# Performance work log

Hardware: AMD Instinct MI355X
Metric: run time of the kernel (lower is better)

The kernel has to match this reference:

```python
import jax, jax.numpy as jnp
import numpy as np

B, CIN, COUT = 2, 32, 32
S = (16, 16, 16, 16)        # input spatial dims
K = (3, 3, 3, 3)            # kernel per spatial dim
PAD = (0, 0, 0, 0)          # conv-transpose padding


def setup_inputs() -> dict:
    key = jax.random.key(0)
    k1, k2, k3 = jax.random.split(key, 3)
    x = jax.random.normal(k1, (B, CIN) + S, dtype=jnp.float32)
    # weight layout mirrors torch ConvTranspose: (in_ch, out_ch, k0, k1, k2, k3)
    # (axis 2 indexes the per-frame sub-convolutions conv_layers[i] of the module)
    weight = jax.random.normal(k2, (CIN, COUT) + K, dtype=jnp.float32) * 0.05
    bias = jax.random.normal(k3, (COUT,), dtype=jnp.float32) * 0.05
    return {"x": x, "weight": weight, "bias": bias}


def _conv_transpose_4d(x, weight, bias):
    # stride-1 conv-transpose == regular conv with spatially flipped kernel
    # and per-side padding (k - 1 - p). This is exactly the math the original
    # module computes via its nested frame-accumulation loops (stride=1).
    w = jnp.flip(weight, axis=(2, 3, 4, 5))          # flip all spatial taps
    w = jnp.transpose(w, (1, 0, 2, 3, 4, 5))         # (O, I, k0..k3)
    pads = [(k - 1 - p, k - 1 - p) for k, p in zip(K, PAD)]
    dn = jax.lax.conv_dimension_numbers(x.shape, w.shape,
                                        ('NCWXYZ', 'OIWXYZ', 'NCWXYZ'))
    y = jax.lax.conv_general_dilated(
        x, w, window_strides=(1, 1, 1, 1), padding=pads,
        dimension_numbers=dn)
    # bias broadcast over batch + 4 spatial dims (module adds per out-channel)
    return y + bias[None, :, None, None, None, None]


def reference(x, weight, bias):
    return _conv_transpose_4d(x, weight, bias)
```

## Files before the change

### kernel.cpp

```cpp
#include <hip/hip_runtime.h>
#include <hip/hip_bf16.h>


#define B_    2
#define CIN_  32
#define SD    16
#define OD    18
#define NTAP  81
#define THREADS 256

typedef unsigned short u16;
typedef __attribute__((ext_vector_type(8))) short short8v;
typedef __attribute__((ext_vector_type(8))) unsigned short u16x8;
typedef __attribute__((ext_vector_type(16))) float f32x16;

__device__ inline u16 f2bf(float f) {
    unsigned u = __float_as_uint(f);
    u = (u + 0x7FFFu + ((u >> 16) & 1u)) >> 16;
    return (u16)u;
}

__device__ inline void decode_o01(int r, int& o0, int& o1) {
    if (r < 196) { o0 = 2 + r / 14; o1 = 2 + r % 14; }
    else if (r < 252) { int q = r - 196;
        if (q < 28) { o0 = 2 + (q >> 1); o1 = (q & 1) ? 16 : 1; }
        else { q -= 28; o1 = 2 + (q >> 1); o0 = (q & 1) ? 16 : 1; } }
    else if (r < 256) { int q = r - 252; o0 = (q & 1) ? 16 : 1; o1 = (q >> 1) ? 16 : 1; }
    else if (r < 312) { int q = r - 256;
        if (q < 28) { o0 = 2 + (q >> 1); o1 = (q & 1) ? 17 : 0; }
        else { q -= 28; o1 = 2 + (q >> 1); o0 = (q & 1) ? 17 : 0; } }
    else if (r < 320) { int q = r - 312;
        if (q < 4) { o0 = (q & 1) ? 16 : 1; o1 = (q >> 1) ? 17 : 0; }
        else { q -= 4; o0 = (q & 1) ? 17 : 0; o1 = (q >> 1) ? 16 : 1; } }
    else { int q = r - 320; o0 = (q & 1) ? 17 : 0; o1 = (q >> 1) ? 17 : 0; }
}

__global__ __launch_bounds__(THREADS)
void prepack_kernel(const float* __restrict__ x, const float* __restrict__ w,
                    u16* __restrict__ xt, u16* __restrict__ wt) {
    const int bid = blockIdx.x, t = threadIdx.x;
    if (bid < 512) {
        const int b = bid >> 8, plane = bid & 255;
        const float* xp = x + (size_t)b * 32 * 65536 + plane * 256 + t;
#pragma unroll
        for (int cg = 0; cg < 4; ++cg) {
            u16x8 v;
#pragma unroll
            for (int j = 0; j < 8; ++j)
                v[j] = f2bf(xp[(size_t)(cg * 8 + j) * 65536]);
            *(u16x8*)(xt + ((size_t)(bid * 4 + cg) * 256 + t) * 8) = v;
        }
    } else {
        const int tap = bid - 512;
#pragma unroll
        for (int q = 0; q < 4; ++q) {
            const int idx = t + q * 256;
            const int ci = idx >> 5, co = idx & 31;
            wt[tap * 1024 + co * 32 + ci] = f2bf(w[((size_t)ci * 32 + co) * NTAP + tap]);
        }
    }
}

__global__ __launch_bounds__(THREADS)
void convt4d_mfma(const u16* __restrict__ xt, const u16* __restrict__ wt,
                  const float* __restrict__ bias, float* __restrict__ y) {
    const int bid = blockIdx.x;
    const int b = bid & 1;
    int o0, o1; decode_o01(bid >> 1, o0, o1);
    const int t = threadIdx.x, l = t & 63, wv = t >> 6;
    const int hi = l >> 5, ln = l & 31;

    const int k0lo = max(0, o0 - (SD - 1)), k0hi = min(2, o0);
    const int k1lo = max(0, o1 - (SD - 1)), k1hi = min(2, o1);

    __shared__ __align__(16) char smem[44032];

    for (int u = t; u < 1600; u += THREADS)
        *(float4*)(smem + u * 16) = make_float4(0.f, 0.f, 0.f, 0.f);

    int tiles[3] = { wv, wv + 4, (wv + 8) % 11 };
    int lpos[3];
#pragma unroll
    for (int mi = 0; mi < 3; ++mi) {
        int p = 32 * tiles[mi] + ln; p = p > 323 ? 323 : p;
        const int o2p = p / 18, o3p = p - o2p * 18;
        lpos[mi] = (o2p + 2) * 20 + o3p + 2;
    }

    f32x16 acc[3];
    { const float bb = bias[ln];
#pragma unroll
      for (int mi = 0; mi < 3; ++mi)
#pragma unroll
        for (int r = 0; r < 16; ++r) acc[mi][r] = bb;
    }

    for (int k0 = k0lo; k0 <= k0hi; ++k0)
    for (int k1 = k1lo; k1 <= k1hi; ++k1) {
        __syncthreads();
        {
            const int plane = (o0 - k0) * 16 + (o1 - k1);
            const u16* src = xt + (size_t)(b * 256 + plane) * 4 * 2048;
#pragma unroll
            for (int q = 0; q < 4; ++q) {
                const int idx = t + q * THREADS;
                const int cg = idx >> 8, pos = idx & 255;
                u16x8 v = *(const u16x8*)(src + (size_t)idx * 8);
                *(u16x8*)(smem + (cg * 400 + ((pos >> 4) + 2) * 20 + (pos & 15) + 2) * 16) = v;
            }
        }
        {
            const u16* srcw = wt + (k0 * 3 + k1) * 9 * 1024;
            for (int idx = t; idx < 1152; idx += THREADS) {
                const int tt = idx >> 7, r = idx & 127, g = r >> 5, co = r & 31;
                u16x8 v = *(const u16x8*)(srcw + tt * 1024 + co * 32 + g * 8);
                *(u16x8*)(smem + 25600 + tt * 2048 + g * 512 + co * 16) = v;
            }
        }
        __syncthreads();

#pragma unroll
        for (int tt = 0; tt < 9; ++tt) {
            const int sh = (tt / 3) * 20 + (tt % 3);
            const int wb = 25600 + tt * 2048 + hi * 512 + ln * 16;
            short8v b0 = *(const short8v*)(smem + wb);
            short8v b1 = *(const short8v*)(smem + wb + 1024);
#pragma unroll
            for (int mi = 0; mi < 3; ++mi) {
                const int ab = (hi * 400 + lpos[mi] - sh) * 16;
                short8v a0 = *(const short8v*)(smem + ab);
                short8v a1 = *(const short8v*)(smem + ab + 12800);
                acc[mi] = __builtin_amdgcn_mfma_f32_32x32x16_bf16(a0, b0, acc[mi], 0, 0, 0);
                acc[mi] = __builtin_amdgcn_mfma_f32_32x32x16_bf16(a1, b1, acc[mi], 0, 0, 0);
            }
        }
    }

    __syncthreads();
#pragma unroll
    for (int mi = 0; mi < 3; ++mi) {
        const int pb = 32 * tiles[mi] + 4 * hi;
#pragma unroll
        for (int r = 0; r < 16; ++r) {
            const int p = pb + (r & 3) + 8 * (r >> 2);
            if (p < 324) *(float*)(smem + (p * 33 + ln) * 4) = acc[mi][r];
        }
    }
    __syncthreads();
    {
        const size_t ybase = (size_t)b * 32 * 104976 + (size_t)(o0 * 18 + o1) * 324;
        for (int co = 0; co < 32; ++co) {
            const float v0 = *(const float*)(smem + (t * 33 + co) * 4);
            y[ybase + (size_t)co * 104976 + t] = v0;
            if (t < 324 - 256) {
                const float v1 = *(const float*)(smem + ((t + 256) * 33 + co) * 4);
                y[ybase + (size_t)co * 104976 + t + 256] = v1;
            }
        }
    }
}

__global__ __launch_bounds__(576, 5)
void convt4d_fp32(const float* __restrict__ x, const float* __restrict__ w,
                  const float* __restrict__ bias, float* __restrict__ y) {
    const int bid = blockIdx.x;
    const int b = bid & 1;
    int o0, o1; decode_o01(bid >> 1, o0, o1);
    const int t = threadIdx.x;
    const int co = t & 15, rr_ = t >> 4, h = rr_ & 1, o2 = rr_ >> 1, i3b = h * 8;
    const int k0lo = max(0, o0 - (SD - 1)), k0hi = min(2, o0);
    const int k1lo = max(0, o1 - (SD - 1)), k1hi = min(2, o1);
    const int n0 = k0hi - k0lo + 1, n1 = k1hi - k1lo + 1;
    __shared__ float4 xs4[2][3][3][64];
    __shared__ float wsl[2 * 32 * NTAP];
    float a0[10], a1[10];
#pragma unroll
    for (int j = 0; j < 10; ++j) { a0[j] = 0.f; a1[j] = 0.f; }
    for (int cc = 0; cc < CIN_; cc += 2) {
        const int total4 = 2 * n0 * n1 * 64;
        for (int idx = t; idx < total4; idx += 576) {
            const int rw = idx >> 6, e = idx & 63;
            const int ci = rw / (n0 * n1), r2 = rw - ci * (n0 * n1);
            const int s0 = r2 / n1, s1 = r2 - s0 * n1;
            const int i0 = o0 - (k0lo + s0), i1 = o1 - (k1lo + s1);
            xs4[ci][s0][s1][e] = ((const float4*)(x +
                ((((size_t)b * CIN_ + (cc + ci)) * SD + i0) * SD + i1) * 256))[e];
        }
        const float4* src = (const float4*)(w + (size_t)cc * 32 * NTAP);
        for (int idx = t; idx < 2 * 32 * NTAP / 4; idx += 576)
            ((float4*)wsl)[idx] = src[idx];
        __syncthreads();
        for (int ci = 0; ci < 2; ++ci)
        for (int s0 = 0; s0 < n0; ++s0)
        for (int s1 = 0; s1 < n1; ++s1) {
            const int k0 = k0lo + s0, k1 = k1lo + s1;
            const float* wp0 = &wsl[(ci * 32 + co) * NTAP + (k0 * 3 + k1) * 9];
            const float* wp1 = wp0 + 16 * NTAP;
            float wv0[9], wv1[9];
#pragma unroll
            for (int q = 0; q < 9; ++q) { wv0[q] = wp0[q]; wv1[q] = wp1[q]; }
            const float* base = (const float*)xs4[ci][s0][s1];
#pragma unroll
            for (int k2 = 0; k2 < 3; ++k2) {
                const int i2 = o2 - k2;
                if ((unsigned)i2 < (unsigned)SD) {
                    const float* xr = base + i2 * SD + i3b;
                    const float4 xa = ((const float4*)xr)[0];
                    const float4 xb = ((const float4*)xr)[1];
                    const float xv[8] = {xa.x, xa.y, xa.z, xa.w, xb.x, xb.y, xb.z, xb.w};
#pragma unroll
                    for (int k3 = 0; k3 < 3; ++k3) {
                        const float c0 = wv0[k2 * 3 + k3], c1 = wv1[k2 * 3 + k3];
#pragma unroll
                        for (int m = 0; m < 8; ++m) {
                            a0[m + k3] += c0 * xv[m]; a1[m + k3] += c1 * xv[m];
                        }
                    }
                }
            }
        }
        __syncthreads();
    }
    float* bnd = (float*)xs4;
    const int slot = (o2 * 16 + co) * 4;
    if (h == 0) { bnd[slot] = a0[8]; bnd[slot + 1] = a0[9]; bnd[slot + 2] = a1[8]; bnd[slot + 3] = a1[9]; }
    __syncthreads();
    const float bb0 = bias[co], bb1 = bias[co + 16];
    float* y0 = y + (((((size_t)b * 32 + co) * OD + o0) * OD + o1) * OD + o2) * OD;
    float* y1 = y0 + (size_t)16 * OD * OD * OD * OD;
    if (h == 0) {
#pragma unroll
        for (int j = 0; j < 4; ++j) {
            ((float2*)y0)[j] = make_float2(a0[2 * j] + bb0, a0[2 * j + 1] + bb0);
            ((float2*)y1)[j] = make_float2(a1[2 * j] + bb1, a1[2 * j + 1] + bb1);
        }
    } else {
        a0[0] += bnd[slot]; a0[1] += bnd[slot + 1]; a1[0] += bnd[slot + 2]; a1[1] += bnd[slot + 3];
#pragma unroll
        for (int j = 0; j < 5; ++j) {
            ((float2*)(y0 + 8))[j] = make_float2(a0[2 * j] + bb0, a0[2 * j + 1] + bb0);
            ((float2*)(y1 + 8))[j] = make_float2(a1[2 * j] + bb1, a1[2 * j + 1] + bb1);
        }
    }
}

extern "C" void kernel_launch(void* const* d_in, const int* in_sizes, int n_in,
                              void* d_out, int out_size, void* d_ws, size_t ws_size,
                              hipStream_t stream) {
    const float* x    = (const float*)d_in[0];
    const float* w    = (const float*)d_in[1];
    const float* bias = (const float*)d_in[2];
    float* y = (float*)d_out;

    const size_t WT_BYTES = 262144;
    const size_t XT_BYTES = (size_t)512 * 4 * 256 * 16;
    if (ws_size >= WT_BYTES + XT_BYTES) {
        u16* wt = (u16*)d_ws;
        u16* xt = (u16*)((char*)d_ws + WT_BYTES);
        prepack_kernel<<<593, THREADS, 0, stream>>>(x, w, xt, wt);
        convt4d_mfma<<<B_ * OD * OD, THREADS, 0, stream>>>(xt, wt, bias, y);
    } else {
        convt4d_fp32<<<B_ * OD * OD, 576, 0, stream>>>(x, w, bias, y);
    }
}
```

Baseline: 112.7 us.

## Prefetch next tap-plane into registers while computing current, prepack weights in LDS layout

The main loop is software-pipelined: the global loads for the next (k0,k1) input plane and weight slice go into registers before the MFMA work on the current slice, and are written to LDS after a barrier. The weight prepack now emits the exact LDS layout, so the in-kernel copy becomes a flat contiguous store, and the prepack grid shrinks from 593 to 521 blocks. MFMA A-operand loads are grouped ahead of the MFMAs. This hides global load latency but holds nine extra vector registers per thread, which may reduce occupancy.

```diff
diff --git a/kernel.cpp b/kernel.cpp
--- a/kernel.cpp
+++ b/kernel.cpp
@@ -51,12 +51,18 @@
             *(u16x8*)(xt + ((size_t)(bid * 4 + cg) * 256 + t) * 8) = v;
         }
     } else {
-        const int tap = bid - 512;
-#pragma unroll
-        for (int q = 0; q < 4; ++q) {
+        const int s = bid - 512;
+#pragma unroll
+        for (int q = 0; q < 5; ++q) {
             const int idx = t + q * 256;
-            const int ci = idx >> 5, co = idx & 31;
-            wt[tap * 1024 + co * 32 + ci] = f2bf(w[((size_t)ci * 32 + co) * NTAP + tap]);
+            if (idx < 1152) {
+                const int tt = idx >> 7, r = idx & 127, g = r >> 5, co = r & 31;
+                u16x8 v;
+#pragma unroll
+                for (int e = 0; e < 8; ++e)
+                    v[e] = f2bf(w[((size_t)(g * 8 + e) * 32 + co) * NTAP + s * 9 + tt]);
+                *(u16x8*)(wt + (size_t)s * 9216 + (size_t)idx * 8) = v;
+            }
         }
     }
 }
@@ -95,29 +101,38 @@
         for (int r = 0; r < 16; ++r) acc[mi][r] = bb;
     }
 
-    for (int k0 = k0lo; k0 <= k0hi; ++k0)
-    for (int k1 = k1lo; k1 <= k1hi; ++k1) {
-        __syncthreads();
-        {
-            const int plane = (o0 - k0) * 16 + (o1 - k1);
-            const u16* src = xt + (size_t)(b * 256 + plane) * 4 * 2048;
-#pragma unroll
-            for (int q = 0; q < 4; ++q) {
-                const int idx = t + q * THREADS;
-                const int cg = idx >> 8, pos = idx & 255;
-                u16x8 v = *(const u16x8*)(src + (size_t)idx * 8);
-                *(u16x8*)(smem + (cg * 400 + ((pos >> 4) + 2) * 20 + (pos & 15) + 2) * 16) = v;
-            }
-        }
-        {
-            const u16* srcw = wt + (k0 * 3 + k1) * 9 * 1024;
-            for (int idx = t; idx < 1152; idx += THREADS) {
-                const int tt = idx >> 7, r = idx & 127, g = r >> 5, co = r & 31;
-                u16x8 v = *(const u16x8*)(srcw + tt * 1024 + co * 32 + g * 8);
-                *(u16x8*)(smem + 25600 + tt * 2048 + g * 512 + co * 16) = v;
-            }
-        }
-        __syncthreads();
+    u16x8 xv[4], wvr[5];
+
+#define PREF(K0, K1) do {                                                      \
+        const int plane_ = (o0 - (K0)) * 16 + (o1 - (K1));                     \
+        const u16* xs_ = xt + (size_t)(b * 256 + plane_) * 8192;               \
+        _Pragma("unroll")                                                      \
+        for (int q = 0; q < 4; ++q) xv[q] = *(const u16x8*)(xs_ + (t + q*256)*8); \
+        const u16* ws_ = wt + (size_t)((K0) * 3 + (K1)) * 9216;                \
+        _Pragma("unroll")                                                      \
+        for (int q = 0; q < 5; ++q) { const int idx_ = t + q*256;              \
+            if (idx_ < 1152) wvr[q] = *(const u16x8*)(ws_ + (size_t)idx_*8); } \
+    } while (0)
+
+#define WRITE() do {                                                           \
+        _Pragma("unroll")                                                      \
+        for (int q = 0; q < 4; ++q)                                            \
+            *(u16x8*)(smem + (q*400 + ((t>>4)+2)*20 + (t&15) + 2) * 16) = xv[q]; \
+        _Pragma("unroll")                                                      \
+        for (int q = 0; q < 5; ++q) { const int idx_ = t + q*256;              \
+            if (idx_ < 1152) *(u16x8*)(smem + 25600 + idx_*16) = wvr[q]; }     \
+    } while (0)
+
+    PREF(k0lo, k1lo);
+    WRITE();
+    __syncthreads();
+
+    int k0 = k0lo, k1 = k1lo;
+    while (true) {
+        int nk0 = k0, nk1 = k1 + 1;
+        if (nk1 > k1hi) { nk0 = k0 + 1; nk1 = k1lo; }
+        const bool has_next = (nk0 <= k0hi);
+        if (has_next) PREF(nk0, nk1);
 
 #pragma unroll
         for (int tt = 0; tt < 9; ++tt) {
@@ -125,18 +140,27 @@
             const int wb = 25600 + tt * 2048 + hi * 512 + ln * 16;
             short8v b0 = *(const short8v*)(smem + wb);
             short8v b1 = *(const short8v*)(smem + wb + 1024);
+            short8v A0[3], A1[3];
 #pragma unroll
             for (int mi = 0; mi < 3; ++mi) {
                 const int ab = (hi * 400 + lpos[mi] - sh) * 16;
-                short8v a0 = *(const short8v*)(smem + ab);
-                short8v a1 = *(const short8v*)(smem + ab + 12800);
-                acc[mi] = __builtin_amdgcn_mfma_f32_32x32x16_bf16(a0, b0, acc[mi], 0, 0, 0);
-                acc[mi] = __builtin_amdgcn_mfma_f32_32x32x16_bf16(a1, b1, acc[mi], 0, 0, 0);
-            }
-        }
-    }
-
-    __syncthreads();
+                A0[mi] = *(const short8v*)(smem + ab);
+                A1[mi] = *(const short8v*)(smem + ab + 12800);
+            }
+#pragma unroll
+            for (int mi = 0; mi < 3; ++mi)
+                acc[mi] = __builtin_amdgcn_mfma_f32_32x32x16_bf16(A0[mi], b0, acc[mi], 0, 0, 0);
+#pragma unroll
+            for (int mi = 0; mi < 3; ++mi)
+                acc[mi] = __builtin_amdgcn_mfma_f32_32x32x16_bf16(A1[mi], b1, acc[mi], 0, 0, 0);
+        }
+        __syncthreads();
+        if (!has_next) break;
+        WRITE();
+        __syncthreads();
+        k0 = nk0; k1 = nk1;
+    }
+
 #pragma unroll
     for (int mi = 0; mi < 3; ++mi) {
         const int pb = 32 * tiles[mi] + 4 * hi;
@@ -158,6 +182,8 @@
             }
         }
     }
+#undef PREF
+#undef WRITE
 }
 
 __global__ __launch_bounds__(576, 5)
@@ -253,11 +279,11 @@
     float* y = (float*)d_out;
 
     const size_t WT_BYTES = 262144;
-    const size_t XT_BYTES = (size_t)512 * 4 * 256 * 16;
+    const size_t XT_BYTES = (size_t)512 * 1024 * 16;
     if (ws_size >= WT_BYTES + XT_BYTES) {
         u16* wt = (u16*)d_ws;
         u16* xt = (u16*)((char*)d_ws + WT_BYTES);
-        prepack_kernel<<<593, THREADS, 0, stream>>>(x, w, xt, wt);
+        prepack_kernel<<<521, THREADS, 0, stream>>>(x, w, xt, wt);
         convt4d_mfma<<<B_ * OD * OD, THREADS, 0, stream>>>(xt, wt, bias, y);
     } else {
         convt4d_fp32<<<B_ * OD * OD, 576, 0, stream>>>(x, w, bias, y);
```

Result: slower. 128.4 us (+13.9%).
